# Kernel optimization log

Hardware: AMD Instinct MI355X
Metric: run time of the kernel (lower is better)

The kernel has to match this reference:

```python
import jax, jax.numpy as jnp
import numpy as np

B, S, H, D = 2, 8192, 16, 64
P = 8            # lsh_num_projs
BS = 256         # block_size
SAMP = 256       # sample_size


def _gray_perm(num_projs):
    # AngularLSH._unit_hamming_distance_array: maps bin ids to Gray-code order
    a = np.array([0, 1], dtype=np.int32)
    for _ in range(num_projs - 1):
        a = np.concatenate([a, np.flip(a) + a.shape[0]])
    return a

_PERM = jnp.asarray(_gray_perm(P))          # (2**P,)
_POW2 = jnp.asarray(2 ** np.arange(P), dtype=jnp.int32)


def setup_inputs() -> dict:
    rng = jax.random.key(0)
    k1, k2, k3, k4, k5 = jax.random.split(rng, 5)
    return {
        "query": jax.random.normal(k1, (B, S, H, D), jnp.float32),
        "key": jax.random.normal(k2, (B, S, H, D), jnp.float32),
        "value": jax.random.normal(k3, (B, S, H, D), jnp.float32),
        "proj_dir": jax.random.normal(k4, (D, P), jnp.float32),
        "sample_idx": jax.random.randint(k5, (B, H, SAMP), 0, S),
    }


def _lsh_hash(x, proj_dir):
    # x: (B,S,H,D) -> Gray-coded bucket ids (B,H,S)
    bits = (jnp.einsum("bshd,dp->bhsp", x, proj_dir) > 0).astype(jnp.int32)
    bins = (bits * _POW2).sum(-1)
    return _PERM[bins]


def _gather_seq(x, idx_bhs):
    # x: (B,S,H,...) gathered along seq by idx (B,H,S)
    idx = jnp.transpose(idx_bhs, (0, 2, 1))  # (B,S,H)
    if x.ndim == 4:
        idx = idx[..., None]
    return jnp.take_along_axis(x, idx, axis=1)


def reference(query, key, value, proj_dir, sample_idx):
    scale = 1.0 / float(np.sqrt(D))
    nb = S // BS

    # --- LSH sort of queries and keys (stable argsort over seq) ---
    q_sort = jnp.argsort(_lsh_hash(query, proj_dir), axis=2)   # (B,H,S)
    k_sort = jnp.argsort(_lsh_hash(key, proj_dir), axis=2)     # (B,H,S)

    q_s = _gather_seq(query, q_sort)   # (B,S,H,D)
    k_s = _gather_seq(key, k_sort)
    v_s = _gather_seq(value, k_sort)

    # --- block-diagonal attention in sorted order ---
    qb = q_s.reshape(B, nb, BS, H, D)
    kb = k_s.reshape(B, nb, BS, H, D)
    vb = v_s.reshape(B, nb, BS, H, D)
    s_blk = jnp.einsum("bnihd,bnjhd->bhnij", qb, kb) * scale   # (B,H,nb,BS,BS)
    lse_blk = jax.nn.logsumexp(s_blk, axis=-1)                 # (B,H,nb,BS)
    a_blk = jnp.einsum("bhnij,bnjhd->bnihd", jax.nn.softmax(s_blk, axis=-1), vb)
    a_blk = a_blk.reshape(B, S, H, D)                          # sorted order
    lse_blk = jnp.transpose(lse_blk, (0, 2, 3, 1)).reshape(B, S, H)

    # un-sort back to original query order
    q_inv = jnp.argsort(q_sort, axis=2)                        # inverse perm (B,H,S)
    a_blk = _gather_seq(a_blk, q_inv)                          # (B,S,H,D)
    lse_blk = _gather_seq(lse_blk, q_inv)                      # (B,S,H)

    # --- residual: uniform sampled-key attention with importance weight ---
    k_r = _gather_seq(key, sample_idx)                         # (B,SAMP,H,D)
    v_r = _gather_seq(value, sample_idx)
    s_r = jnp.einsum("bihd,bjhd->bhij", query, k_r) * scale    # (B,H,S,SAMP)
    lse_r = jax.nn.logsumexp(s_r, axis=-1) + jnp.log(S / SAMP) # (B,H,S)
    a_r = jnp.einsum("bhij,bjhd->bihd", jax.nn.softmax(s_r, axis=-1), v_r)
    lse_r = jnp.transpose(lse_r, (0, 2, 1))                    # (B,S,H)

    # --- combine block + residual estimates via log-sum-exp ---
    lse_t = jnp.logaddexp(lse_blk, lse_r)                      # (B,S,H)
    w_blk = jnp.exp(lse_blk - lse_t)[..., None]
    w_r = jnp.exp(lse_r - lse_t)[..., None]
    attn = a_blk * w_blk + a_r * w_r                           # (B,S,H,D)
    return attn
```

## Files before the change

### kernel.cpp

```cpp
#include <hip/hip_runtime.h>
#include <hip/hip_bf16.h>

#define B 2
#define S 8192
#define H 16
#define D 64
#define NB 32
#define BS 256
#define SAMP 256
#define BH (B*H)
#define BHS (B*H*S)
#define BSHD (B*S*H*D)
#define LOG32 3.4657359027997265f

typedef float f32x4 __attribute__((ext_vector_type(4)));
typedef short bf16x8 __attribute__((ext_vector_type(8)));

__device__ __forceinline__ unsigned int pack2(float a, float b) {
    unsigned int r;
    asm("v_cvt_pk_bf16_f32 %0, %1, %2" : "=v"(r) : "v"(a), "v"(b));
    return r;
}

#define HP 34

__global__ __launch_bounds__(256, 3) void k_hash(const float* __restrict__ q,
                                                 const float* __restrict__ k,
                                                 const float* __restrict__ pd,
                                                 int* __restrict__ hq,
                                                 int* __restrict__ hk,
                                                 unsigned short* __restrict__ kbf) {
    __shared__ float spd4[4 * 520];
    __shared__ unsigned int tile[256 * HP];
    __shared__ int ht[16][16];
    const int t = threadIdx.x;
    for (int i = t; i < 512; i += 256) {
        const float val = pd[i];
        spd4[i] = val; spd4[520 + i] = val;
        spd4[1040 + i] = val; spd4[1560 + i] = val;
    }
    __syncthreads();

    const bool isK = blockIdx.x >= 1024;
    const int  blk = blockIdx.x & 1023;
    const float* src = isK ? k : q;
    int* hdst = isK ? hk : hq;

    const int lane = t & 63;
    const int c    = lane & 3;
    const int rql  = (t >> 6) * 64 + (lane >> 2) * 4;
    const int rowq = blk * 256 + rql;
    const float* sp = spd4 + c * 520;

    float d[4][8];
#pragma unroll
    for (int rr = 0; rr < 4; ++rr)
#pragma unroll
        for (int p = 0; p < 8; ++p) d[rr][p] = 0.f;

#pragma unroll
    for (int j = 0; j < 4; ++j) {
        float4 x[4];
#pragma unroll
        for (int rr = 0; rr < 4; ++rr)
            x[rr] = *(const float4*)(src + ((rowq + rr) << 6) + j * 16 + c * 4);

        if (isK) {
#pragma unroll
            for (int rr = 0; rr < 4; ++rr) {
                uint2 u2;
                u2.x = pack2(x[rr].x, x[rr].y);
                u2.y = pack2(x[rr].z, x[rr].w);
                *(uint2*)&tile[(rql + rr) * HP + j * 8 + c * 2] = u2;
            }
        }
#pragma unroll
        for (int u = 0; u < 4; ++u) {
            const int dim = j * 16 + c * 4 + u;
            float4 s0 = *(const float4*)&sp[dim * 8];
            float4 s1 = *(const float4*)&sp[dim * 8 + 4];
#pragma unroll
            for (int rr = 0; rr < 4; ++rr) {
                const float xv = (u == 0) ? x[rr].x : (u == 1) ? x[rr].y
                               : (u == 2) ? x[rr].z : x[rr].w;
                d[rr][0] += xv * s0.x; d[rr][1] += xv * s0.y;
                d[rr][2] += xv * s0.z; d[rr][3] += xv * s0.w;
                d[rr][4] += xv * s1.x; d[rr][5] += xv * s1.y;
                d[rr][6] += xv * s1.z; d[rr][7] += xv * s1.w;
            }
        }
    }
#pragma unroll
    for (int rr = 0; rr < 4; ++rr)
#pragma unroll
        for (int p = 0; p < 8; ++p) {
            d[rr][p] += __shfl_xor(d[rr][p], 1);
            d[rr][p] += __shfl_xor(d[rr][p], 2);
        }
    int bits[4];
#pragma unroll
    for (int rr = 0; rr < 4; ++rr) {
        int bv = 0;
#pragma unroll
        for (int p = 0; p < 8; ++p) bv |= (d[rr][p] > 0.f) ? (1 << p) : 0;
        bits[rr] = bv;
    }
    const int myb = (c == 0) ? bits[0] : (c == 1) ? bits[1]
                  : (c == 2) ? bits[2] : bits[3];
    const int myrl = rql + c;
    ht[myrl & 15][myrl >> 4] = myb ^ (myb >> 1);
    __syncthreads();

    if (isK) {
        uint4* dst = (uint4*)(kbf + blk * 256 * 64);
#pragma unroll
        for (int it = 0; it < 8; ++it) {
            const int g = it * 256 + t;
            const unsigned int* sl = &tile[(g >> 3) * HP + (g & 7) * 4];
            uint4 val;
            val.x = sl[0]; val.y = sl[1]; val.z = sl[2]; val.w = sl[3];
            dst[g] = val;
        }
    }
    if (t < 64) {
        const int h2 = t >> 2, p2 = t & 3;
        int4 val = *(const int4*)&ht[h2][p2 * 4];
        const int gb = blk >> 9;
        const int s0 = (blk * 16) & (S - 1);
        *(int4*)&hdst[(gb * H + h2) * S + s0 + p2 * 4] = val;
    }
}

#define SORT_NT 64
#define SORT_CH (S / SORT_NT)

__global__ __launch_bounds__(SORT_NT) void k_sort(const int* __restrict__ hq,
                                                  const int* __restrict__ hk,
                                                  int* __restrict__ qs,
                                                  int* __restrict__ ks) {
    __shared__ int hist[SORT_NT * 256];
    __shared__ int base[257];
    const int t  = threadIdx.x;
    const int bh = blockIdx.x & (BH - 1);
    const bool isQ = blockIdx.x < BH;
    const int* hp = (isQ ? hq : hk) + bh * S;
    int*       sp = (isQ ? qs : ks) + bh * S;

    for (int i = 0; i < 256; ++i) hist[t * 256 + i] = 0;
    __syncthreads();
    for (int i = 0; i < SORT_CH; ++i) hist[t * 256 + hp[t * SORT_CH + i]]++;
    __syncthreads();

    int v0 = 0, v1 = 0, v2 = 0, v3 = 0;
    for (int tt = 0; tt < SORT_NT; ++tt) {
        const int* hr = &hist[tt * 256 + t * 4];
        v0 += hr[0]; v1 += hr[1]; v2 += hr[2]; v3 += hr[3];
    }
    {
        const int s1 = v0 + v1, s2 = s1 + v2, tot = s2 + v3;
        int inc = tot;
#pragma unroll
        for (int dlt = 1; dlt < 64; dlt <<= 1) {
            const int n = __shfl_up(inc, dlt);
            if (t >= dlt) inc += n;
        }
        const int ex = inc - tot;
        base[4 * t + 1] = ex + v0;
        base[4 * t + 2] = ex + s1;
        base[4 * t + 3] = ex + s2;
        base[4 * t + 4] = ex + tot;
        if (t == 0) base[0] = 0;
    }
    __syncthreads();

    for (int bi = 0; bi < 4; ++bi) {
        const int bin = t * 4 + bi;
        int run = base[bin];
        for (int tt = 0; tt < SORT_NT; ++tt) {
            int c = hist[tt * 256 + bin];
            hist[tt * 256 + bin] = run;
            run += c;
        }
    }
    __syncthreads();

    for (int i = 0; i < SORT_CH; ++i) {
        const int s0  = t * SORT_CH + i;
        const int bin = hp[s0];
        sp[hist[t * 256 + bin]++] = s0;
    }
}

#define VP 264
#define PP 40

__global__ __launch_bounds__(512, 2) void k_attn(const float* __restrict__ q,
                                                 const unsigned short* __restrict__ kbf,
                                                 const float* __restrict__ v,
                                                 const int* __restrict__ qs,
                                                 const int* __restrict__ ks,
                                                 const int* __restrict__ sidx,
                                                 float* __restrict__ out) {
    __shared__ __align__(16) unsigned short vT[64 * VP];
    __shared__ __align__(16) unsigned short pL[8 * 32 * PP];

    const int t    = threadIdx.x;
    const int w    = t >> 6;
    const int lane = t & 63;
    const int lg   = lane >> 4;
    const int lr   = lane & 15;
    const int logical = (blockIdx.x & 7) * (BH * NB / 8) + (blockIdx.x >> 3);
    const int blk  = logical & (NB - 1);
    const int bh   = logical >> 5;
    const int h    = bh & (H - 1), b = bh >> 4;
    const int sbase = bh * S + blk * BS;
    unsigned short* pw = pL + w * 32 * PP;

    int qrow[2]; bf16x8 bq[2][2];
#pragma unroll
    for (int qg = 0; qg < 2; ++qg) {
        qrow[qg] = qs[sbase + w * 32 + qg * 16 + lr];
        const float* qp = q + (((b * S + qrow[qg]) * H + h) << 6);
#pragma unroll
        for (int kf = 0; kf < 2; ++kf) {
            float4 x0 = ((const float4*)(qp + kf * 32 + lg * 8))[0];
            float4 x1 = ((const float4*)(qp + kf * 32 + lg * 8))[1];
            union { bf16x8 v8; unsigned int u[4]; } fa;
            fa.u[0] = pack2(x0.x * 0.125f, x0.y * 0.125f);
            fa.u[1] = pack2(x0.z * 0.125f, x0.w * 0.125f);
            fa.u[2] = pack2(x1.x * 0.125f, x1.y * 0.125f);
            fa.u[3] = pack2(x1.z * 0.125f, x1.w * 0.125f);
            bq[qg][kf] = fa.v8;
        }
    }

    float m_run[2] = {-1e30f, -1e30f}, l_run[2] = {0.f, 0.f};
    f32x4 acc[2][4];
#pragma unroll
    for (int qg = 0; qg < 2; ++qg)
#pragma unroll
        for (int dg = 0; dg < 4; ++dg) acc[qg][dg] = (f32x4){0.f, 0.f, 0.f, 0.f};

    for (int pass = 0; pass < 2; ++pass) {
        {
            const int key = t & 255, d0 = (t >> 8) * 32;
            const int krow = pass ? sidx[bh * SAMP + key] : ks[sbase + key];
            const float* vp = v + (((b * S + krow) * H + h) << 6) + d0;
            unsigned int uv[16];
#pragma unroll
            for (int i = 0; i < 8; ++i) {
                float4 y = ((const float4*)vp)[i];
                uv[2 * i]     = pack2(y.x, y.y);
                uv[2 * i + 1] = pack2(y.z, y.w);
            }
            if (pass) __syncthreads();
#pragma unroll
            for (int j = 0; j < 16; ++j) {
                const int d = d0 + 2 * j;
                vT[(d + 0) * VP + key] = (unsigned short)(uv[j]);
                vT[(d + 1) * VP + key] = (unsigned short)(uv[j] >> 16);
            }
        }
        __syncthreads();

        const float bias = pass ? LOG32 : 0.f;

        int krw[4]; bf16x8 akp[4];
#pragma unroll
        for (int kg = 0; kg < 4; ++kg) {
            const int key = kg * 16 + lr;
            krw[kg] = pass ? sidx[bh * SAMP + key] : ks[sbase + key];
        }
#pragma unroll
        for (int kg = 0; kg < 4; ++kg)
            akp[kg] = *(const bf16x8*)(kbf + (((b * S + krw[kg]) * H + h) << 6) + lg * 8);

#pragma unroll
        for (int kt4 = 0; kt4 < 4; ++kt4) {
            bf16x8 ak1[4];
#pragma unroll
            for (int kg = 0; kg < 4; ++kg)
                ak1[kg] = *(const bf16x8*)(kbf + (((b * S + krw[kg]) * H + h) << 6)
                                           + 32 + lg * 8);
            f32x4 c[2][4];
            __builtin_amdgcn_s_setprio(1);
#pragma unroll
            for (int qg = 0; qg < 2; ++qg)
#pragma unroll
                for (int kg = 0; kg < 4; ++kg) {
                    f32x4 z = (f32x4){0.f, 0.f, 0.f, 0.f};
                    z = __builtin_amdgcn_mfma_f32_16x16x32_bf16(akp[kg], bq[qg][0], z, 0, 0, 0);
                    c[qg][kg] = __builtin_amdgcn_mfma_f32_16x16x32_bf16(ak1[kg], bq[qg][1], z, 0, 0, 0);
                }
            __builtin_amdgcn_s_setprio(0);

            int krwn[4]; bf16x8 akn[4];
            if (kt4 < 3) {
#pragma unroll
                for (int kg = 0; kg < 4; ++kg) {
                    const int key = (kt4 + 1) * 64 + kg * 16 + lr;
                    krwn[kg] = pass ? sidx[bh * SAMP + key] : ks[sbase + key];
                }
#pragma unroll
                for (int kg = 0; kg < 4; ++kg)
                    akn[kg] = *(const bf16x8*)(kbf + (((b * S + krwn[kg]) * H + h) << 6)
                                               + lg * 8);
            }

#pragma unroll
            for (int qg = 0; qg < 2; ++qg) {
                float tm = -1e30f;
#pragma unroll
                for (int kg = 0; kg < 4; ++kg)
#pragma unroll
                    for (int r = 0; r < 4; ++r) tm = fmaxf(tm, c[qg][kg][r]);
                tm = fmaxf(tm, __shfl_xor(tm, 16));
                tm = fmaxf(tm, __shfl_xor(tm, 32));
                tm += bias;
                if (!__all(tm <= m_run[qg] + 8.f)) {
                    const float mn  = fmaxf(m_run[qg], tm);
                    const float es  = __expf(m_run[qg] - mn);
                    m_run[qg] = mn;
                    l_run[qg] *= es;
#pragma unroll
                    for (int r = 0; r < 4; ++r) {
                        const float er = __shfl(es, lg * 4 + r);
#pragma unroll
                        for (int dg = 0; dg < 4; ++dg) acc[qg][dg][r] *= er;
                    }
                }
                const float mnb = m_run[qg] - bias;
                float rs = 0.f;
#pragma unroll
                for (int kg = 0; kg < 4; ++kg)
#pragma unroll
                    for (int r = 0; r < 4; ++r) {
                        const float p = __expf(c[qg][kg][r] - mnb);
                        c[qg][kg][r] = p;
                        rs += p;
                    }
                rs += __shfl_xor(rs, 16);
                rs += __shfl_xor(rs, 32);
                l_run[qg] += rs;
            }
#pragma unroll
            for (int hh = 0; hh < 2; ++hh) {
#pragma unroll
                for (int qg = 0; qg < 2; ++qg)
#pragma unroll
                    for (int kg2 = 0; kg2 < 2; ++kg2) {
                        const int kg = hh * 2 + kg2;
                        uint2 u;
                        u.x = pack2(c[qg][kg][0], c[qg][kg][1]);
                        u.y = pack2(c[qg][kg][2], c[qg][kg][3]);
                        *(uint2*)&pw[(qg * 16 + lr) * PP + kg2 * 16 + lg * 4] = u;
                    }
                bf16x8 bv[4];
#pragma unroll
                for (int dg = 0; dg < 4; ++dg)
                    bv[dg] = *(const bf16x8*)&vT[(dg * 16 + lr) * VP + kt4 * 64 + hh * 32 + lg * 8];
                bf16x8 ap[2];
#pragma unroll
                for (int qg = 0; qg < 2; ++qg)
                    ap[qg] = *(const bf16x8*)&pw[(qg * 16 + lr) * PP + lg * 8];
                __builtin_amdgcn_s_setprio(1);
#pragma unroll
                for (int qg = 0; qg < 2; ++qg)
#pragma unroll
                    for (int dg = 0; dg < 4; ++dg)
                        acc[qg][dg] = __builtin_amdgcn_mfma_f32_16x16x32_bf16(ap[qg], bv[dg], acc[qg][dg], 0, 0, 0);
                __builtin_amdgcn_s_setprio(0);
            }

            if (kt4 < 3) {
#pragma unroll
                for (int kg = 0; kg < 4; ++kg) { krw[kg] = krwn[kg]; akp[kg] = akn[kg]; }
            }
        }
    }

#pragma unroll
    for (int qg = 0; qg < 2; ++qg)
#pragma unroll
        for (int r = 0; r < 4; ++r) {
            const float lq = __shfl(l_run[qg], lg * 4 + r);
            const int   qr = __shfl(qrow[qg], lg * 4 + r);
            const float inv = 1.f / lq;
            const int obase = ((b * S + qr) * H + h) << 6;
#pragma unroll
            for (int dg = 0; dg < 4; ++dg)
                out[obase + dg * 16 + lr] = acc[qg][dg][r] * inv;
        }
}

extern "C" void kernel_launch(void* const* d_in, const int* in_sizes, int n_in,
                              void* d_out, int out_size, void* d_ws, size_t ws_size,
                              hipStream_t stream) {
    const float* q   = (const float*)d_in[0];
    const float* k   = (const float*)d_in[1];
    const float* v   = (const float*)d_in[2];
    const float* pd  = (const float*)d_in[3];
    const int*  sidx = (const int*)d_in[4];
    float* out = (float*)d_out;

    int* hq = (int*)d_ws;
    int* hk = hq + BHS;
    int* qs = hk + BHS;
    int* ks = qs + BHS;
    unsigned short* kbf = (unsigned short*)(ks + BHS);

    k_hash<<<2048, 256, 0, stream>>>(q, k, pd, hq, hk, kbf);
    k_sort<<<2 * BH, SORT_NT, 0, stream>>>(hq, hk, qs, ks);
    k_attn<<<BH * NB, 512, 0, stream>>>(q, kbf, v, qs, ks, sidx, out);
}
```

Measured before the change: 191.2 us.

## Compute softmax row sums via extra MFMA with ones column; pad sort histogram

Replaces the per-tile scalar row-sum of exponentials and its cross-lane shuffle reductions with an extra MFMA per query group that multiplies the bf16 probabilities by a ones column, accumulating the normaliser in matrix-core registers and rescaling it with the accumulator. Also pads the sort kernel's per-thread histogram pitch to 257 to avoid LDS bank conflicts. The ones-MFMA sums bf16-rounded probabilities, which slightly changes numerics, and adds MFMA work and accumulator registers.

New measurement: 188.8 us, median of 2. No clear change (-1.3%).

```diff
diff --git a/kernel.cpp b/kernel.cpp
--- a/kernel.cpp
+++ b/kernel.cpp
@@ -133,12 +133,13 @@
 
 #define SORT_NT 64
 #define SORT_CH (S / SORT_NT)
+#define HPitch 257
 
 __global__ __launch_bounds__(SORT_NT) void k_sort(const int* __restrict__ hq,
                                                   const int* __restrict__ hk,
                                                   int* __restrict__ qs,
                                                   int* __restrict__ ks) {
-    __shared__ int hist[SORT_NT * 256];
+    __shared__ int hist[SORT_NT * HPitch];
     __shared__ int base[257];
     const int t  = threadIdx.x;
     const int bh = blockIdx.x & (BH - 1);
@@ -146,14 +147,14 @@
     const int* hp = (isQ ? hq : hk) + bh * S;
     int*       sp = (isQ ? qs : ks) + bh * S;
 
-    for (int i = 0; i < 256; ++i) hist[t * 256 + i] = 0;
-    __syncthreads();
-    for (int i = 0; i < SORT_CH; ++i) hist[t * 256 + hp[t * SORT_CH + i]]++;
+    for (int i = 0; i < HPitch; ++i) hist[t * HPitch + i] = 0;
+    __syncthreads();
+    for (int i = 0; i < SORT_CH; ++i) hist[t * HPitch + hp[t * SORT_CH + i]]++;
     __syncthreads();
 
     int v0 = 0, v1 = 0, v2 = 0, v3 = 0;
     for (int tt = 0; tt < SORT_NT; ++tt) {
-        const int* hr = &hist[tt * 256 + t * 4];
+        const int* hr = &hist[tt * HPitch + t * 4];
         v0 += hr[0]; v1 += hr[1]; v2 += hr[2]; v3 += hr[3];
     }
     {
@@ -177,8 +178,8 @@
         const int bin = t * 4 + bi;
         int run = base[bin];
         for (int tt = 0; tt < SORT_NT; ++tt) {
-            int c = hist[tt * 256 + bin];
-            hist[tt * 256 + bin] = run;
+            int c = hist[tt * HPitch + bin];
+            hist[tt * HPitch + bin] = run;
             run += c;
         }
     }
@@ -187,7 +188,7 @@
     for (int i = 0; i < SORT_CH; ++i) {
         const int s0  = t * SORT_CH + i;
         const int bin = hp[s0];
-        sp[hist[t * 256 + bin]++] = s0;
+        sp[hist[t * HPitch + bin]++] = s0;
     }
 }
 
@@ -234,12 +235,23 @@
         }
     }
 
-    float m_run[2] = {-1e30f, -1e30f}, l_run[2] = {0.f, 0.f};
+    bf16x8 bv5;
+    {
+        union { bf16x8 v8; unsigned int u[4]; } fo;
+        const unsigned int ov = (lr == 0) ? 0x3F803F80u : 0u;
+        fo.u[0] = ov; fo.u[1] = ov; fo.u[2] = ov; fo.u[3] = ov;
+        bv5 = fo.v8;
+    }
+
+    float m_run[2] = {-1e30f, -1e30f};
     f32x4 acc[2][4];
-#pragma unroll
-    for (int qg = 0; qg < 2; ++qg)
+    f32x4 acc5[2];
+#pragma unroll
+    for (int qg = 0; qg < 2; ++qg) {
+        acc5[qg] = (f32x4){0.f, 0.f, 0.f, 0.f};
 #pragma unroll
         for (int dg = 0; dg < 4; ++dg) acc[qg][dg] = (f32x4){0.f, 0.f, 0.f, 0.f};
+    }
 
     for (int pass = 0; pass < 2; ++pass) {
         {
@@ -321,27 +333,20 @@
                     const float mn  = fmaxf(m_run[qg], tm);
                     const float es  = __expf(m_run[qg] - mn);
                     m_run[qg] = mn;
-                    l_run[qg] *= es;
 #pragma unroll
                     for (int r = 0; r < 4; ++r) {
                         const float er = __shfl(es, lg * 4 + r);
 #pragma unroll
                         for (int dg = 0; dg < 4; ++dg) acc[qg][dg][r] *= er;
+                        acc5[qg][r] *= er;
                     }
                 }
                 const float mnb = m_run[qg] - bias;
-                float rs = 0.f;
 #pragma unroll
                 for (int kg = 0; kg < 4; ++kg)
 #pragma unroll
-                    for (int r = 0; r < 4; ++r) {
-                        const float p = __expf(c[qg][kg][r] - mnb);
-                        c[qg][kg][r] = p;
-                        rs += p;
-                    }
-                rs += __shfl_xor(rs, 16);
-                rs += __shfl_xor(rs, 32);
-                l_run[qg] += rs;
+                    for (int r = 0; r < 4; ++r)
+                        c[qg][kg][r] = __expf(c[qg][kg][r] - mnb);
             }
 #pragma unroll
             for (int hh = 0; hh < 2; ++hh) {
@@ -365,10 +370,12 @@
                     ap[qg] = *(const bf16x8*)&pw[(qg * 16 + lr) * PP + lg * 8];
                 __builtin_amdgcn_s_setprio(1);
 #pragma unroll
-                for (int qg = 0; qg < 2; ++qg)
+                for (int qg = 0; qg < 2; ++qg) {
 #pragma unroll
                     for (int dg = 0; dg < 4; ++dg)
                         acc[qg][dg] = __builtin_amdgcn_mfma_f32_16x16x32_bf16(ap[qg], bv[dg], acc[qg][dg], 0, 0, 0);
+                    acc5[qg] = __builtin_amdgcn_mfma_f32_16x16x32_bf16(ap[qg], bv5, acc5[qg], 0, 0, 0);
+                }
                 __builtin_amdgcn_s_setprio(0);
             }
 
@@ -383,7 +390,7 @@
     for (int qg = 0; qg < 2; ++qg)
 #pragma unroll
         for (int r = 0; r < 4; ++r) {
-            const float lq = __shfl(l_run[qg], lg * 4 + r);
+            const float lq = __shfl(acc5[qg][r], lg * 16);
             const int   qr = __shfl(qrow[qg], lg * 4 + r);
             const float inv = 1.f / lq;
             const int obase = ((b * S + qr) * H + h) << 6;
```
